# Performance work log

Measured on AMD Instinct MI355X. Metric: run time of the kernel, lower is better.

Reference implementation:

```python
import jax, jax.numpy as jnp
import numpy as np

EPS = 1e-5

def adain_norm(x):
    # per-(batch,channel) instance normalization over spatial dims (AdaIN projection)
    mean = jnp.mean(x, axis=(2, 3), keepdims=True)
    var = jnp.var(x, axis=(2, 3), keepdims=True)
    return (x - mean) / jnp.sqrt(var + EPS)

def conv1x1(x, w, b):
    # x: [B,C,H,W], w: [O,C], b: [O]
    return jnp.einsum('bchw,oc->bohw', x, w) + b[None, :, None, None]

def setup_inputs() -> dict:
    key = jax.random.key(0)
    ks = jax.random.split(key, 10)
    B, C, H, W = 4, 512, 64, 64
    s = 1.0 / np.sqrt(C)
    return {
        'x': jax.random.normal(ks[0], (B, C, H, W), jnp.float32),
        'y': jax.random.normal(ks[1], (B, C, H, W), jnp.float32),
        'f_w': jax.random.normal(ks[2], (C, C), jnp.float32) * s,
        'f_b': jnp.zeros((C,), jnp.float32),
        'g_w': jax.random.normal(ks[3], (C, C), jnp.float32) * s,
        'g_b': jnp.zeros((C,), jnp.float32),
        'h_w': jax.random.normal(ks[4], (C, C), jnp.float32) * s,
        'h_b': jnp.zeros((C,), jnp.float32),
        'out_w': jax.random.normal(ks[5], (C, C), jnp.float32) * s,
        'out_b': jnp.zeros((C,), jnp.float32),
    }

def reference(x, y, f_w, f_b, g_w, g_b, h_w, h_b, out_w, out_b):
    B, C, H, W = x.shape
    HW = H * W
    xn = adain_norm(x)
    yn = adain_norm(y)
    # 1x1 conv projections, flattened over spatial dims
    f = conv1x1(xn, f_w, f_b).reshape(B, C, HW)   # [B,C,HWx]
    g = conv1x1(yn, g_w, g_b).reshape(B, C, HW)   # [B,C,HWy]
    energy = jnp.einsum('bci,bcj->bij', f, g)     # [B,HWx,HWy]
    correlation = jax.nn.softmax(energy, axis=-1)
    h = conv1x1(y, h_w, h_b).reshape(B, C, HW)    # [B,C,HWy]
    # residual = h @ correlation^T -> [B,C,HWx]
    residual = jnp.einsum('bcj,bij->bci', h, correlation).reshape(B, C, H, W)
    residual = conv1x1(residual, out_w, out_b)
    return x + residual
```

## Files before the change

### kernel.cpp

```cpp
#include <hip/hip_runtime.h>
#include <stdint.h>

#define HW 4096
#define NC 512
#define NB 4

typedef __attribute__((ext_vector_type(8))) _Float16 f16x8;
typedef __attribute__((ext_vector_type(4))) float f32x4;
typedef __attribute__((ext_vector_type(4))) unsigned short ush4;
typedef __attribute__((ext_vector_type(8))) unsigned short ush8;

typedef __attribute__((address_space(1))) const void* as1_cvp;
typedef __attribute__((address_space(3))) void* as3_vp;

__device__ __forceinline__ unsigned short f2h(float f) {
  union { _Float16 h; unsigned short u; } c;
  c.h = (_Float16)f;
  return c.u;
}
__device__ __forceinline__ float h2f(unsigned short u) {
  union { unsigned short u; _Float16 h; } c;
  c.u = u;
  return (float)c.h;
}

__global__ __launch_bounds__(256) void moments_k(const float* __restrict__ x,
                                                 const float* __restrict__ y,
                                                 float* __restrict__ stats) {
  int bid = blockIdx.x;
  int tens = bid >> 11;
  int row = bid & 2047;
  const float* src = (tens ? y : x) + (size_t)row * HW;
  float s = 0.f, s2 = 0.f;
  for (int j = threadIdx.x; j < HW / 4; j += 256) {
    float4 v = ((const float4*)src)[j];
    s += (v.x + v.y) + (v.z + v.w);
    s2 += (v.x * v.x + v.y * v.y) + (v.z * v.z + v.w * v.w);
  }
  #pragma unroll
  for (int o = 32; o; o >>= 1) { s += __shfl_down(s, o); s2 += __shfl_down(s2, o); }
  __shared__ float rs[8];
  int w = threadIdx.x >> 6;
  if ((threadIdx.x & 63) == 0) { rs[w] = s; rs[4 + w] = s2; }
  __syncthreads();
  if (threadIdx.x == 0) {
    float S = (rs[0] + rs[1]) + (rs[2] + rs[3]);
    float S2 = (rs[4] + rs[5]) + (rs[6] + rs[7]);
    float mean = S * (1.f / HW);
    float var = S2 * (1.f / HW) - mean * mean;
    stats[tens * 4096 + row] = mean;
    stats[tens * 4096 + 2048 + row] = rsqrtf(var + 1e-5f);
  }
}

__global__ __launch_bounds__(256) void transnorm_k(const float* __restrict__ x,
                                                   const float* __restrict__ y,
                                                   const float* __restrict__ stats,
                                                   unsigned short* __restrict__ xnT,
                                                   unsigned short* __restrict__ ynT,
                                                   unsigned short* __restrict__ yT) {
  __shared__ float tile[64][65];
  __shared__ float ms[64], rsd[64];
  int zi = blockIdx.z;
  int b = zi >> 1, mode = zi & 1;
  int i0 = blockIdx.x * 64, c0 = blockIdx.y * 64;
  const float* src = mode ? y : x;
  int t = threadIdx.x;
  int c = t >> 2;
  int isub = (t & 3) << 4;
  if (t < 64) {
    int srow = (mode ? 4096 : 0) + b * NC + c0 + t;
    ms[t] = stats[srow];
    rsd[t] = stats[srow + 2048];
  }
  const float4* sp = (const float4*)(src + ((size_t)(b * NC + c0 + c)) * HW + i0 + isub);
  #pragma unroll
  for (int k = 0; k < 4; ++k) {
    float4 v = sp[k];
    int ib = isub + k * 4;
    tile[ib + 0][c] = v.x;
    tile[ib + 1][c] = v.y;
    tile[ib + 2][c] = v.z;
    tile[ib + 3][c] = v.w;
  }
  __syncthreads();
  int i = t >> 2;
  int cc = (t & 3) << 4;
  size_t obase = ((size_t)b * HW + i0 + i) * NC + c0 + cc;
  if (mode == 0) {
    #pragma unroll
    for (int h = 0; h < 2; ++h) {
      ush8 o;
      #pragma unroll
      for (int e = 0; e < 8; ++e) {
        int ce = cc + h * 8 + e;
        o[e] = f2h((tile[i][ce] - ms[ce]) * rsd[ce]);
      }
      *(ush8*)(xnT + obase + h * 8) = o;
    }
  } else {
    #pragma unroll
    for (int h = 0; h < 2; ++h) {
      ush8 on,or_;
      #pragma unroll
      for (int e = 0; e < 8; ++e) {
        int ce = cc + h * 8 + e;
        float raw = tile[i][ce];
        on[e] = f2h((raw - ms[ce]) * rsd[ce]);
        or_[e] = f2h(raw);
      }
      *(ush8*)(ynT + obase + h * 8) = on;
      *(ush8*)(yT + obase + h * 8) = or_;
    }
  }
}

__global__ __launch_bounds__(256) void castw_k(const float* __restrict__ fw,
                                               const float* __restrict__ gw,
                                               const float* __restrict__ hw_,
                                               const float* __restrict__ ow,
                                               unsigned short* __restrict__ dst) {
  int idx = blockIdx.x * 256 + threadIdx.x;
  int which = idx >> 16;
  int sub = idx & 65535;
  const float* s = which == 0 ? fw : which == 1 ? gw : which == 2 ? hw_ : ow;
  float4 v = ((const float4*)s)[sub];
  ush4 o;
  o[0] = f2h(v.x); o[1] = f2h(v.y); o[2] = f2h(v.z); o[3] = f2h(v.w);
  *(ush4*)(dst + (size_t)idx * 4) = o;
}

__global__ __launch_bounds__(256) void softmax_h(unsigned short* __restrict__ S) {
  unsigned short* row = S + (size_t)blockIdx.x * HW;
  int t = threadIdx.x;
  ush8 a0 = *(const ush8*)(row + t * 16);
  ush8 a1 = *(const ush8*)(row + t * 16 + 8);
  float v[16];
  #pragma unroll
  for (int e = 0; e < 8; ++e) { v[e] = h2f(a0[e]); v[8 + e] = h2f(a1[e]); }
  float mx = -3.0e38f;
  #pragma unroll
  for (int e = 0; e < 16; ++e) mx = fmaxf(mx, v[e]);
  #pragma unroll
  for (int o = 32; o; o >>= 1) mx = fmaxf(mx, __shfl_down(mx, o));
  __shared__ float red[8];
  int w = t >> 6;
  if ((t & 63) == 0) red[w] = mx;
  __syncthreads();
  mx = fmaxf(fmaxf(red[0], red[1]), fmaxf(red[2], red[3]));
  float sum = 0.f;
  #pragma unroll
  for (int e = 0; e < 16; ++e) { v[e] = __expf(v[e] - mx); sum += v[e]; }
  #pragma unroll
  for (int o = 32; o; o >>= 1) sum += __shfl_down(sum, o);
  if ((t & 63) == 0) red[4 + w] = sum;
  __syncthreads();
  float inv = 1.f / ((red[4] + red[5]) + (red[6] + red[7]));
  ush8 o0, o1;
  #pragma unroll
  for (int e = 0; e < 8; ++e) { o0[e] = f2h(v[e] * inv); o1[e] = f2h(v[8 + e] * inv); }
  *(ush8*)(row + t * 16) = o0;
  *(ush8*)(row + t * 16 + 8) = o1;
}

__global__ __launch_bounds__(256) void reduce_k(const float* __restrict__ P4,
                                                unsigned short* __restrict__ op,
                                                long long PSo, int R, int pzs) {
  int e = blockIdx.x * 256 + threadIdx.x;
  int bg = e >> pzs;
  int rem = e - (bg << pzs);
  const float4* base = (const float4*)P4 + ((size_t)bg * 4) * R * (NC / 4) + rem;
  float4 s = {0.f, 0.f, 0.f, 0.f};
  #pragma unroll
  for (int sp = 0; sp < 4; ++sp) {
    float4 v = base[(size_t)sp * R * (NC / 4)];
    s.x += v.x; s.y += v.y; s.z += v.z; s.w += v.w;
  }
  int m = rem >> 7, c4 = rem & 127;
  ush4 o;
  o[0] = f2h(s.x); o[1] = f2h(s.y); o[2] = f2h(s.z); o[3] = f2h(s.w);
  *(ush4*)(op + (size_t)bg * PSo + (size_t)m * NC + c4 * 4) = o;
}

__global__ __launch_bounds__(256, 2) void gemm_ntp(
    const unsigned short* __restrict__ A, long long sA, int lda,
    const unsigned short* __restrict__ Bm, long long sB, int ldb,
    void* __restrict__ Cp, long long sC, long long sCs, int ldc,
    int K, int out_f32, int ls,
    const float* __restrict__ bias_m, const float* __restrict__ bias_n,
    const float* __restrict__ add_src, long long sAdd,
    const unsigned short* __restrict__ B2, const float* __restrict__ bias_n2,
    int zsw) {
  __shared__ short lsA[2][128 * 64];
  __shared__ short lsB[2][128 * 64];
  const int t = threadIdx.x;
  const int lane = t & 63;
  const int w = t >> 6;
  const int wm = w >> 1, wn = w & 1;
  const long long bz = blockIdx.z;
  if ((int)bz >= zsw) { Bm = B2; bias_n = bias_n2; }
  const long long bg = bz >> ls;
  const int sp = (int)(bz - (bg << ls));
  const long long koff = (long long)sp * K;
  const unsigned short* Ab = A + bz * sA * (ls ? 0 : 1) + (ls ? bg * sA : 0) + koff
                           + (size_t)blockIdx.x * 128 * lda;
  const unsigned short* Bb = Bm + bg * sB + koff + (size_t)blockIdx.y * 128 * ldb;

  f32x4 zero = {0.f, 0.f, 0.f, 0.f};
  f32x4 acc[4][4];
  #pragma unroll
  for (int i = 0; i < 4; ++i)
    #pragma unroll
    for (int j = 0; j < 4; ++j) acc[i][j] = zero;

  const int nkt = K >> 6;

  auto STAGE = [&](int buf, int kt) {
    const int kbase = kt << 6;
    #pragma unroll
    for (int i = 0; i < 4; ++i) {
      int q = t + i * 256;
      int r = q >> 3, xx = q & 7;
      int gk = kbase + ((xx ^ (r & 7)) << 3);
      __builtin_amdgcn_global_load_lds((as1_cvp)(const void*)(Ab + (size_t)r * lda + gk),
                                       (as3_vp)(void*)(&lsA[buf][q << 3]), 16, 0, 0);
      __builtin_amdgcn_global_load_lds((as1_cvp)(const void*)(Bb + (size_t)r * ldb + gk),
                                       (as3_vp)(void*)(&lsB[buf][q << 3]), 16, 0, 0);
    }
  };

  STAGE(0, 0);
  __syncthreads();
  int cur = 0;
  for (int kt = 0; kt < nkt; ++kt) {
    if (kt + 1 < nkt) STAGE(cur ^ 1, kt + 1);
    #pragma unroll
    for (int ks = 0; ks < 2; ++ks) {
      f16x8 av[4], bv[4];
      const int xl = ks * 4 + (lane >> 4);
      const int rr = lane & 15;
      #pragma unroll
      for (int mb = 0; mb < 4; ++mb) {
        int row = wm * 64 + mb * 16 + rr;
        av[mb] = *(const f16x8*)&lsA[cur][(row << 6) + ((xl ^ (row & 7)) << 3)];
      }
      #pragma unroll
      for (int nb = 0; nb < 4; ++nb) {
        int row = wn * 64 + nb * 16 + rr;
        bv[nb] = *(const f16x8*)&lsB[cur][(row << 6) + ((xl ^ (row & 7)) << 3)];
      }
      __builtin_amdgcn_s_setprio(1);
      #pragma unroll
      for (int mb = 0; mb < 4; ++mb)
        #pragma unroll
        for (int nb = 0; nb < 4; ++nb)
          acc[mb][nb] = __builtin_amdgcn_mfma_f32_16x16x32_f16(av[mb], bv[nb], acc[mb][nb], 0, 0, 0);
      __builtin_amdgcn_s_setprio(0);
    }
    __syncthreads();
    cur ^= 1;
  }

  const int mb0 = blockIdx.x * 128 + wm * 64;
  const int nb0 = blockIdx.y * 128 + wn * 64;
  const int cn = lane & 15;
  const int rq = (lane >> 4) << 2;
  float* cf = (float*)Cp;
  unsigned short* ch = (unsigned short*)Cp;
  #pragma unroll
  for (int mb = 0; mb < 4; ++mb) {
    #pragma unroll
    for (int nb = 0; nb < 4; ++nb) {
      int n = nb0 + nb * 16 + cn;
      float bn = bias_n ? bias_n[n] : 0.f;
      #pragma unroll
      for (int r = 0; r < 4; ++r) {
        int m = mb0 + mb * 16 + rq + r;
        float vv = acc[mb][nb][r] + bn;
        if (bias_m) vv += bias_m[m];
        if (add_src) vv += add_src[bg * sAdd + (size_t)m * ldc + n];
        size_t off = (size_t)(bg * sC) + (size_t)sp * sCs + (size_t)m * ldc + n;
        if (out_f32) cf[off] = vv;
        else ch[off] = f2h(vv);
      }
    }
  }
}

__global__ __launch_bounds__(512, 2) void gemm_nt2(
    const unsigned short* __restrict__ A, long long sA, int lda,
    const unsigned short* __restrict__ Bm, long long sB, int ldb,
    void* __restrict__ Cp, long long sC, int ldc,
    int K, int out_f32) {
  __shared__ short lsA[2][256 * 64];
  __shared__ short lsB[2][256 * 64];
  const int t = threadIdx.x;
  const int lane = t & 63;
  const int w = t >> 6;
  const int wm = w >> 2, wn = w & 3;
  const long long bz = blockIdx.z;
  const unsigned short* Ab = A + bz * sA + (size_t)blockIdx.x * 256 * lda;
  const unsigned short* Bb = Bm + bz * sB + (size_t)blockIdx.y * 256 * ldb;

  f32x4 zero = {0.f, 0.f, 0.f, 0.f};
  f32x4 acc[8][4];
  #pragma unroll
  for (int i = 0; i < 8; ++i)
    #pragma unroll
    for (int j = 0; j < 4; ++j) acc[i][j] = zero;

  const int rr = lane & 15;
  const int xl = lane >> 4;
  const int nkt = K >> 6;

  auto STAGE = [&](int buf, int kt) {
    const int kbase = kt << 6;
    #pragma unroll
    for (int i = 0; i < 4; ++i) {
      int q = t + i * 512;
      int r = q >> 3, xx = q & 7;
      int gk = kbase + ((xx ^ (r & 7)) << 3);
      __builtin_amdgcn_global_load_lds((as1_cvp)(const void*)(Ab + (size_t)r * lda + gk),
                                       (as3_vp)(void*)(&lsA[buf][q << 3]), 16, 0, 0);
      __builtin_amdgcn_global_load_lds((as1_cvp)(const void*)(Bb + (size_t)r * ldb + gk),
                                       (as3_vp)(void*)(&lsB[buf][q << 3]), 16, 0, 0);
    }
  };

  STAGE(0, 0);
  __syncthreads();
  int cur = 0;
  for (int kt = 0; kt < nkt; ++kt) {
    if (kt + 1 < nkt) STAGE(cur ^ 1, kt + 1);
    #pragma unroll
    for (int ks = 0; ks < 2; ++ks) {
      f16x8 av[8], bv[4];
      const int cb = ks * 4 + xl;
      #pragma unroll
      for (int mb = 0; mb < 8; ++mb) {
        int row = wm * 128 + mb * 16 + rr;
        av[mb] = *(const f16x8*)&lsA[cur][(row << 6) + ((cb ^ (row & 7)) << 3)];
      }
      #pragma unroll
      for (int nb = 0; nb < 4; ++nb) {
        int row = wn * 64 + nb * 16 + rr;
        bv[nb] = *(const f16x8*)&lsB[cur][(row << 6) + ((cb ^ (row & 7)) << 3)];
      }
      __builtin_amdgcn_s_setprio(1);
      #pragma unroll
      for (int mb = 0; mb < 8; ++mb)
        #pragma unroll
        for (int nb = 0; nb < 4; ++nb)
          acc[mb][nb] = __builtin_amdgcn_mfma_f32_16x16x32_f16(av[mb], bv[nb], acc[mb][nb], 0, 0, 0);
      __builtin_amdgcn_s_setprio(0);
    }
    __syncthreads();
    cur ^= 1;
  }

  const int mb0 = blockIdx.x * 256 + wm * 128;
  const int nb0 = blockIdx.y * 256 + wn * 64;
  const int cn = lane & 15;
  const int rq = (lane >> 4) << 2;
  float* cf = (float*)Cp;
  unsigned short* ch = (unsigned short*)Cp;
  #pragma unroll
  for (int mb = 0; mb < 8; ++mb) {
    #pragma unroll
    for (int nb = 0; nb < 4; ++nb) {
      int n = nb0 + nb * 16 + cn;
      #pragma unroll
      for (int r = 0; r < 4; ++r) {
        int m = mb0 + mb * 16 + rq + r;
        float vv = acc[mb][nb][r];
        size_t off = (size_t)(bz * sC) + (size_t)m * ldc + n;
        if (out_f32) cf[off] = vv;
        else ch[off] = f2h(vv);
      }
    }
  }
}

extern "C" void kernel_launch(void* const* d_in, const int* in_sizes, int n_in,
                              void* d_out, int out_size, void* d_ws, size_t ws_size,
                              hipStream_t stream) {
  const float* x = (const float*)d_in[0];
  const float* y = (const float*)d_in[1];
  const float* f_w = (const float*)d_in[2];
  const float* f_b = (const float*)d_in[3];
  const float* g_w = (const float*)d_in[4];
  const float* g_b = (const float*)d_in[5];
  const float* h_w = (const float*)d_in[6];
  const float* h_b = (const float*)d_in[7];
  const float* out_w = (const float*)d_in[8];
  const float* out_b = (const float*)d_in[9];
  float* out = (float*)d_out;

  char* ws = (char*)d_ws;
  size_t off = 0;
  auto alloc = [&](size_t bytes) -> char* {
    char* p = ws + off;
    off += (bytes + 255) & ~(size_t)255;
    return p;
  };
  const size_t TN = (size_t)NB * HW * NC;
  float* stats = (float*)alloc(8192 * sizeof(float));
  unsigned short* wB = (unsigned short*)alloc((size_t)4 * 512 * 512 * 2);
  unsigned short* xnT = (unsigned short*)alloc(TN * 2);
  unsigned short* ynT = (unsigned short*)alloc(TN * 2);
  unsigned short* yT = (unsigned short*)alloc(TN * 2);
  unsigned short* fB = (unsigned short*)alloc(TN * 2);
  unsigned short* gB = (unsigned short*)alloc(TN * 2);
  unsigned short* hB = (unsigned short*)alloc(TN * 2);
  unsigned short* oB = xnT;
  size_t remain = ws_size > off ? ws_size - off : 0;
  const size_t SB = (size_t)HW * HW * 2 + (size_t)4 * HW * NC * 4;
  int G, R = HW;
  if (remain >= 4 * SB)      { G = 4; }
  else if (remain >= 2 * SB) { G = 2; }
  else if (remain >= SB)     { G = 1; }
  else {
    G = 1;
    while (R > 128 && (size_t)R * (HW * 2 + 16 * NC) > remain) R >>= 1;
  }
  unsigned short* Sh = (unsigned short*)alloc((size_t)G * R * HW * 2);
  float* P4 = (float*)alloc((size_t)G * 4 * R * NC * 4);
  if (off > ws_size) return;

  castw_k<<<dim3(1024), dim3(256), 0, stream>>>(f_w, g_w, h_w, out_w, wB);
  moments_k<<<dim3(4096), dim3(256), 0, stream>>>(x, y, stats);
  transnorm_k<<<dim3(64, 8, 8), dim3(256), 0, stream>>>(x, y, stats, xnT, ynT, yT);

  const long long PS = (long long)HW * NC;
  const int BIG = 1 << 30;
  gemm_ntp<<<dim3(32, 4, 8), dim3(256), 0, stream>>>(
      xnT, PS, NC, wB, 0, NC, fB, PS, 0, NC, NC, 0, 0,
      nullptr, f_b, nullptr, 0, wB + 262144, g_b, 4);
  gemm_ntp<<<dim3(4, 32, NB), dim3(256), 0, stream>>>(
      wB + 524288, 0, NC, yT, PS, NC, hB, PS, 0, HW, NC, 0, 0,
      h_b, nullptr, nullptr, 0, nullptr, nullptr, BIG);

  const int pzs = 31 - __builtin_clz((unsigned)(R * (NC / 4)));
  for (int b0 = 0; b0 < NB; b0 += G) {
    for (int r0 = 0; r0 < HW; r0 += R) {
      if (R >= 256) {
        gemm_nt2<<<dim3(R / 256, HW / 256, G), dim3(512), 0, stream>>>(
            fB + ((size_t)b0 * HW + r0) * NC, PS, NC,
            gB + (size_t)b0 * PS, PS, NC,
            Sh, (long long)R * HW, HW, NC, 0);
      } else {
        gemm_ntp<<<dim3(R / 128, 32, G), dim3(256), 0, stream>>>(
            fB + ((size_t)b0 * HW + r0) * NC, PS, NC,
            gB + (size_t)b0 * PS, PS, NC,
            Sh, (long long)R * HW, 0, HW, NC, 0, 0,
            nullptr, nullptr, nullptr, 0, nullptr, nullptr, BIG);
      }
      softmax_h<<<dim3(G * R), dim3(256), 0, stream>>>(Sh);
      gemm_ntp<<<dim3(R / 128, 4, G * 4), dim3(256), 0, stream>>>(
          Sh, (long long)R * HW, HW,
          hB + (size_t)b0 * NC * HW, (long long)NC * HW, HW,
          P4, (long long)4 * R * NC, (long long)R * NC, NC, HW / 4, 1, 2,
          nullptr, nullptr, nullptr, 0, nullptr, nullptr, BIG);
      reduce_k<<<dim3(G * R / 2), dim3(256), 0, stream>>>(
          P4, oB + ((size_t)b0 * HW + r0) * NC, PS, R, pzs);
    }
  }
  gemm_ntp<<<dim3(4, 32, NB), dim3(256), 0, stream>>>(
      wB + 786432, 0, NC, oB, PS, NC,
      out, (long long)NC * HW, 0, HW, NC, 1, 0,
      out_b, nullptr, x, (long long)NC * HW, nullptr, nullptr, BIG);
}
```

Measured before the change: 407.5 us.

## Fold f/g and h/out weight products algebraically to drop two projection GEMMs

Rewrites energy = xn·Wf^T·Wg·yn as xn·(Wg^T Wf)^T·yn, so a single precomputed 512x512 matrix replaces the separate g projection. The f bias only adds a per-column term, which is computed as a dot product and added as a column bias in the energy GEMM; the g bias is dropped because it is constant along the softmax axis. Likewise the h projection is folded into the output conv (W2 = out_w·h_w, b2 = out_b + out_w·h_b), since softmax rows sum to one, so attention runs directly on fp16 y. This removes two full-size projection GEMMs and their intermediate buffers at the cost of small weight-product GEMMs and extra fp16 rounding of the combined weights.

```diff
diff --git a/kernel.cpp b/kernel.cpp
--- a/kernel.cpp
+++ b/kernel.cpp
@@ -58,7 +58,7 @@
                                                    const float* __restrict__ stats,
                                                    unsigned short* __restrict__ xnT,
                                                    unsigned short* __restrict__ ynT,
-                                                   unsigned short* __restrict__ yT) {
+                                                   unsigned short* __restrict__ yH) {
   __shared__ float tile[64][65];
   __shared__ float ms[64], rsd[64];
   int zi = blockIdx.z;
@@ -82,36 +82,26 @@
     tile[ib + 1][c] = v.y;
     tile[ib + 2][c] = v.z;
     tile[ib + 3][c] = v.w;
+    if (mode) {
+      ush4 yo;
+      yo[0] = f2h(v.x); yo[1] = f2h(v.y); yo[2] = f2h(v.z); yo[3] = f2h(v.w);
+      *(ush4*)(yH + ((size_t)(b * NC + c0 + c)) * HW + i0 + isub + k * 4) = yo;
+    }
   }
   __syncthreads();
   int i = t >> 2;
   int cc = (t & 3) << 4;
   size_t obase = ((size_t)b * HW + i0 + i) * NC + c0 + cc;
-  if (mode == 0) {
-    #pragma unroll
-    for (int h = 0; h < 2; ++h) {
-      ush8 o;
-      #pragma unroll
-      for (int e = 0; e < 8; ++e) {
-        int ce = cc + h * 8 + e;
-        o[e] = f2h((tile[i][ce] - ms[ce]) * rsd[ce]);
-      }
-      *(ush8*)(xnT + obase + h * 8) = o;
-    }
-  } else {
-    #pragma unroll
-    for (int h = 0; h < 2; ++h) {
-      ush8 on,or_;
-      #pragma unroll
-      for (int e = 0; e < 8; ++e) {
-        int ce = cc + h * 8 + e;
-        float raw = tile[i][ce];
-        on[e] = f2h((raw - ms[ce]) * rsd[ce]);
-        or_[e] = f2h(raw);
-      }
-      *(ush8*)(ynT + obase + h * 8) = on;
-      *(ush8*)(yT + obase + h * 8) = or_;
-    }
+  unsigned short* dst = mode ? ynT : xnT;
+  #pragma unroll
+  for (int h = 0; h < 2; ++h) {
+    ush8 o;
+    #pragma unroll
+    for (int e = 0; e < 8; ++e) {
+      int ce = cc + h * 8 + e;
+      o[e] = f2h((tile[i][ce] - ms[ce]) * rsd[ce]);
+    }
+    *(ush8*)(dst + obase + h * 8) = o;
   }
 }
 
@@ -119,15 +109,79 @@
                                                const float* __restrict__ gw,
                                                const float* __restrict__ hw_,
                                                const float* __restrict__ ow,
-                                               unsigned short* __restrict__ dst) {
-  int idx = blockIdx.x * 256 + threadIdx.x;
-  int which = idx >> 16;
-  int sub = idx & 65535;
-  const float* s = which == 0 ? fw : which == 1 ? gw : which == 2 ? hw_ : ow;
-  float4 v = ((const float4*)s)[sub];
-  ush4 o;
-  o[0] = f2h(v.x); o[1] = f2h(v.y); o[2] = f2h(v.z); o[3] = f2h(v.w);
-  *(ush4*)(dst + (size_t)idx * 4) = o;
+                                               unsigned short* __restrict__ fwT,
+                                               unsigned short* __restrict__ gwT,
+                                               unsigned short* __restrict__ hwT,
+                                               unsigned short* __restrict__ owB) {
+  __shared__ float tile[64][65];
+  int which = blockIdx.z;
+  const float* src = which == 0 ? fw : which == 1 ? gw : which == 2 ? hw_ : ow;
+  unsigned short* dst = which == 0 ? fwT : which == 1 ? gwT : which == 2 ? hwT : owB;
+  int r0 = blockIdx.x * 64, c0 = blockIdx.y * 64;
+  int t = threadIdx.x;
+  int r = t >> 2;
+  int csub = (t & 3) << 4;
+  const float4* sp = (const float4*)(src + (size_t)(r0 + r) * 512 + c0 + csub);
+  if (which == 3) {
+    #pragma unroll
+    for (int k = 0; k < 4; ++k) {
+      float4 v = sp[k];
+      ush4 o;
+      o[0] = f2h(v.x); o[1] = f2h(v.y); o[2] = f2h(v.z); o[3] = f2h(v.w);
+      *(ush4*)(dst + (size_t)(r0 + r) * 512 + c0 + csub + k * 4) = o;
+    }
+    return;
+  }
+  #pragma unroll
+  for (int k = 0; k < 4; ++k) {
+    float4 v = sp[k];
+    int cb = csub + k * 4;
+    tile[cb + 0][r] = v.x;
+    tile[cb + 1][r] = v.y;
+    tile[cb + 2][r] = v.z;
+    tile[cb + 3][r] = v.w;
+  }
+  __syncthreads();
+  int cw = t >> 2;
+  int rsub = (t & 3) << 4;
+  #pragma unroll
+  for (int h = 0; h < 2; ++h) {
+    ush8 o;
+    #pragma unroll
+    for (int e = 0; e < 8; ++e) o[e] = f2h(tile[cw][rsub + h * 8 + e]);
+    *(ush8*)(dst + (size_t)(c0 + cw) * 512 + r0 + rsub + h * 8) = o;
+  }
+}
+
+__global__ __launch_bounds__(256) void dotrows_h(const unsigned short* __restrict__ A,
+                                                 const float* __restrict__ vec,
+                                                 float* __restrict__ out) {
+  int row = blockIdx.x * 4 + (threadIdx.x >> 6);
+  int lane = threadIdx.x & 63;
+  ush8 a = *(const ush8*)(A + (size_t)row * 512 + lane * 8);
+  float s = 0.f;
+  #pragma unroll
+  for (int e = 0; e < 8; ++e) s += h2f(a[e]) * vec[lane * 8 + e];
+  #pragma unroll
+  for (int o = 32; o; o >>= 1) s += __shfl_down(s, o);
+  if (lane == 0) out[row] = s;
+}
+
+__global__ __launch_bounds__(256) void b2_k(const float* __restrict__ Wf,
+                                            const float* __restrict__ hb,
+                                            const float* __restrict__ ob,
+                                            float* __restrict__ out) {
+  int row = blockIdx.x * 4 + (threadIdx.x >> 6);
+  int lane = threadIdx.x & 63;
+  const float4* a = (const float4*)(Wf + (size_t)row * 512) + lane * 2;
+  float4 x0 = a[0], x1 = a[1];
+  const float4* hv = (const float4*)hb + lane * 2;
+  float4 h0 = hv[0], h1 = hv[1];
+  float s = x0.x * h0.x + x0.y * h0.y + x0.z * h0.z + x0.w * h0.w
+          + x1.x * h1.x + x1.y * h1.y + x1.z * h1.z + x1.w * h1.w;
+  #pragma unroll
+  for (int o = 32; o; o >>= 1) s += __shfl_down(s, o);
+  if (lane == 0) out[row] = ob[row] + s;
 }
 
 __global__ __launch_bounds__(256) void softmax_h(unsigned short* __restrict__ S) {
@@ -291,7 +345,8 @@
     const unsigned short* __restrict__ A, long long sA, int lda,
     const unsigned short* __restrict__ Bm, long long sB, int ldb,
     void* __restrict__ Cp, long long sC, int ldc,
-    int K, int out_f32) {
+    int K, int out_f32,
+    const float* __restrict__ bias_n, long long sBn) {
   __shared__ short lsA[2][256 * 64];
   __shared__ short lsB[2][256 * 64];
   const int t = threadIdx.x;
@@ -369,10 +424,11 @@
     #pragma unroll
     for (int nb = 0; nb < 4; ++nb) {
       int n = nb0 + nb * 16 + cn;
+      float bn = bias_n ? bias_n[bz * sBn + n] : 0.f;
       #pragma unroll
       for (int r = 0; r < 4; ++r) {
         int m = mb0 + mb * 16 + rq + r;
-        float vv = acc[mb][nb][r];
+        float vv = acc[mb][nb][r] + bn;
         size_t off = (size_t)(bz * sC) + (size_t)m * ldc + n;
         if (out_f32) cf[off] = vv;
         else ch[off] = f2h(vv);
@@ -395,6 +451,7 @@
   const float* out_w = (const float*)d_in[8];
   const float* out_b = (const float*)d_in[9];
   float* out = (float*)d_out;
+  (void)g_b;
 
   char* ws = (char*)d_ws;
   size_t off = 0;
@@ -404,14 +461,21 @@
     return p;
   };
   const size_t TN = (size_t)NB * HW * NC;
+  const size_t WN = (size_t)512 * 512;
   float* stats = (float*)alloc(8192 * sizeof(float));
-  unsigned short* wB = (unsigned short*)alloc((size_t)4 * 512 * 512 * 2);
+  unsigned short* fwT = (unsigned short*)alloc(WN * 2);
+  unsigned short* gwT = (unsigned short*)alloc(WN * 2);
+  unsigned short* hwT = (unsigned short*)alloc(WN * 2);
+  unsigned short* owB = (unsigned short*)alloc(WN * 2);
+  unsigned short* W1T = (unsigned short*)alloc(WN * 2);
+  unsigned short* W2 = (unsigned short*)alloc(WN * 2);
+  float* vv = (float*)alloc(512 * 4);
+  float* b2 = (float*)alloc(512 * 4);
+  float* wj = (float*)alloc((size_t)NB * HW * 4);
   unsigned short* xnT = (unsigned short*)alloc(TN * 2);
   unsigned short* ynT = (unsigned short*)alloc(TN * 2);
-  unsigned short* yT = (unsigned short*)alloc(TN * 2);
+  unsigned short* yH = (unsigned short*)alloc(TN * 2);
   unsigned short* fB = (unsigned short*)alloc(TN * 2);
-  unsigned short* gB = (unsigned short*)alloc(TN * 2);
-  unsigned short* hB = (unsigned short*)alloc(TN * 2);
   unsigned short* oB = xnT;
   size_t remain = ws_size > off ? ws_size - off : 0;
   const size_t SB = (size_t)HW * HW * 2 + (size_t)4 * HW * NC * 4;
@@ -427,18 +491,26 @@
   float* P4 = (float*)alloc((size_t)G * 4 * R * NC * 4);
   if (off > ws_size) return;
 
-  castw_k<<<dim3(1024), dim3(256), 0, stream>>>(f_w, g_w, h_w, out_w, wB);
-  moments_k<<<dim3(4096), dim3(256), 0, stream>>>(x, y, stats);
-  transnorm_k<<<dim3(64, 8, 8), dim3(256), 0, stream>>>(x, y, stats, xnT, ynT, yT);
-
   const long long PS = (long long)HW * NC;
   const int BIG = 1 << 30;
-  gemm_ntp<<<dim3(32, 4, 8), dim3(256), 0, stream>>>(
-      xnT, PS, NC, wB, 0, NC, fB, PS, 0, NC, NC, 0, 0,
-      nullptr, f_b, nullptr, 0, wB + 262144, g_b, 4);
-  gemm_ntp<<<dim3(4, 32, NB), dim3(256), 0, stream>>>(
-      wB + 524288, 0, NC, yT, PS, NC, hB, PS, 0, HW, NC, 0, 0,
-      h_b, nullptr, nullptr, 0, nullptr, nullptr, BIG);
+
+  castw_k<<<dim3(8, 8, 4), dim3(256), 0, stream>>>(f_w, g_w, h_w, out_w,
+                                                   fwT, gwT, hwT, owB);
+  moments_k<<<dim3(4096), dim3(256), 0, stream>>>(x, y, stats);
+  transnorm_k<<<dim3(64, 8, 8), dim3(256), 0, stream>>>(x, y, stats, xnT, ynT, yH);
+
+  dotrows_h<<<dim3(128), dim3(256), 0, stream>>>(gwT, f_b, vv);
+  b2_k<<<dim3(128), dim3(256), 0, stream>>>(out_w, h_b, out_b, b2);
+  gemm_ntp<<<dim3(4, 4, 1), dim3(256), 0, stream>>>(
+      gwT, 0, 512, fwT, 0, 512, W1T, 0, 0, 512, 512, 0, 0,
+      nullptr, nullptr, nullptr, 0, nullptr, nullptr, BIG);
+  gemm_ntp<<<dim3(4, 4, 1), dim3(256), 0, stream>>>(
+      owB, 0, 512, hwT, 0, 512, W2, 0, 0, 512, 512, 0, 0,
+      nullptr, nullptr, nullptr, 0, nullptr, nullptr, BIG);
+  dotrows_h<<<dim3(NB * HW / 4), dim3(256), 0, stream>>>(ynT, vv, wj);
+  gemm_ntp<<<dim3(32, 4, NB), dim3(256), 0, stream>>>(
+      xnT, PS, NC, W1T, 0, NC, fB, PS, 0, NC, NC, 0, 0,
+      nullptr, nullptr, nullptr, 0, nullptr, nullptr, BIG);
 
   const int pzs = 31 - __builtin_clz((unsigned)(R * (NC / 4)));
   for (int b0 = 0; b0 < NB; b0 += G) {
@@ -446,19 +518,20 @@
       if (R >= 256) {
         gemm_nt2<<<dim3(R / 256, HW / 256, G), dim3(512), 0, stream>>>(
             fB + ((size_t)b0 * HW + r0) * NC, PS, NC,
-            gB + (size_t)b0 * PS, PS, NC,
-            Sh, (long long)R * HW, HW, NC, 0);
+            ynT + (size_t)b0 * PS, PS, NC,
+            Sh, (long long)R * HW, HW, NC, 0,
+            wj + (size_t)b0 * HW, HW);
       } else {
         gemm_ntp<<<dim3(R / 128, 32, G), dim3(256), 0, stream>>>(
             fB + ((size_t)b0 * HW + r0) * NC, PS, NC,
-            gB + (size_t)b0 * PS, PS, NC,
+            ynT + (size_t)b0 * PS, PS, NC,
             Sh, (long long)R * HW, 0, HW, NC, 0, 0,
-            nullptr, nullptr, nullptr, 0, nullptr, nullptr, BIG);
+            nullptr, wj + (size_t)b0 * HW, nullptr, 0, nullptr, nullptr, BIG);
       }
       softmax_h<<<dim3(G * R), dim3(256), 0, stream>>>(Sh);
       gemm_ntp<<<dim3(R / 128, 4, G * 4), dim3(256), 0, stream>>>(
           Sh, (long long)R * HW, HW,
-          hB + (size_t)b0 * NC * HW, (long long)NC * HW, HW,
+          yH + (size_t)b0 * NC * HW, (long long)NC * HW, HW,
           P4, (long long)4 * R * NC, (long long)R * NC, NC, HW / 4, 1, 2,
           nullptr, nullptr, nullptr, 0, nullptr, nullptr, BIG);
       reduce_k<<<dim3(G * R / 2), dim3(256), 0, stream>>>(
@@ -466,7 +539,7 @@
     }
   }
   gemm_ntp<<<dim3(4, 32, NB), dim3(256), 0, stream>>>(
-      wB + 786432, 0, NC, oB, PS, NC,
+      W2, 0, NC, oB, PS, NC,
       out, (long long)NC * HW, 0, HW, NC, 1, 0,
-      out_b, nullptr, x, (long long)NC * HW, nullptr, nullptr, BIG);
-}
+      b2, nullptr, x, (long long)NC * HW, nullptr, nullptr, BIG);
+}
```

Measured after the change: 407.2 us. No clear change (-0.1%).
